# Optimization experiments

Hardware: AMD Instinct MI355X
Metric: run time of the kernel (lower is better)

Reference implementation:

```python
import jax, jax.numpy as jnp
import numpy as np
import math

B, T, F, H, C = 64, 128, 2048, 1024, 22

def setup_inputs() -> dict:
    key = jax.random.key(0)
    ks = jax.random.split(key, 16)
    def w(k, shape, fan_in):
        s = 1.0 / math.sqrt(fan_in)
        return jax.random.uniform(k, shape, jnp.float32, -s, s)
    return {
        "x": jax.random.normal(ks[0], (B, T, F), jnp.float32),
        # encoder LSTM (input F, hidden H); PyTorch gate order i,f,g,o
        "enc_Wih": w(ks[1], (4 * H, F), H),
        "enc_Whh": w(ks[2], (4 * H, H), H),
        "enc_bih": w(ks[3], (4 * H,), H),
        "enc_bhh": w(ks[4], (4 * H,), H),
        # enc->dec and dec->enc projections (both HxH, unidirectional)
        "We2d": w(ks[5], (H, H), H),
        "be2d": w(ks[6], (H,), H),
        "Wd2e": w(ks[7], (H, H), H),
        "bd2e": w(ks[8], (H,), H),
        # decoder LSTMCell (input F + H, hidden H)
        "dec_Wih": w(ks[9], (4 * H, F + H), H),
        "dec_Whh": w(ks[10], (4 * H, H), H),
        "dec_bih": w(ks[11], (4 * H,), H),
        "dec_bhh": w(ks[12], (4 * H,), H),
        # classifier
        "Wc": w(ks[13], (C, H), H),
        "bc": w(ks[14], (C,), H),
    }

def _lstm_cell(x_t, h, c, Wih, Whh, b):
    g = x_t @ Wih.T + h @ Whh.T + b  # [B, 4H]
    i, f, gg, o = jnp.split(g, 4, axis=-1)
    c_new = jax.nn.sigmoid(f) * c + jax.nn.sigmoid(i) * jnp.tanh(gg)
    h_new = jax.nn.sigmoid(o) * jnp.tanh(c_new)
    return h_new, c_new

def reference(x, enc_Wih, enc_Whh, enc_bih, enc_bhh, We2d, be2d, Wd2e, bd2e,
              dec_Wih, dec_Whh, dec_bih, dec_bhh, Wc, bc):
    Bx, Tx, _ = x.shape
    Hh = enc_Whh.shape[1]
    enc_b = enc_bih + enc_bhh
    dec_b = dec_bih + dec_bhh

    # ---- encoder LSTM over time (feature extractor is identity) ----
    xT = jnp.swapaxes(x, 0, 1)  # [T, B, F]
    def enc_step(carry, x_t):
        h, c = carry
        h, c = _lstm_cell(x_t, h, c, enc_Wih, enc_Whh, enc_b)
        return (h, c), h
    h0 = jnp.zeros((Bx, Hh), x.dtype)
    (_, _), h_ts = jax.lax.scan(enc_step, (h0, h0), xT)  # [T, B, H]
    h_ts = jnp.swapaxes(h_ts, 0, 1)  # [B, T, H]

    proj_h_ts = h_ts @ We2d.T + be2d  # [B, T, H]
    scale = 1.0 / math.sqrt(Hh)

    # ---- decoder with per-step attention ----
    def dec_step(carry, x_t):
        h, c = carry
        logits = jnp.einsum('bh,bth->bt', h, proj_h_ts) * scale
        aw = jax.nn.softmax(logits, axis=-1)           # [B, T]
        attn = jnp.einsum('bt,bth->bh', aw, proj_h_ts)  # [B, H]
        attn = attn @ Wd2e.T + bd2e
        inp = jnp.concatenate([x_t, attn], axis=-1)     # [B, F+H]
        h, c = _lstm_cell(inp, h, c, dec_Wih, dec_Whh, dec_b)
        sc = h @ Wc.T + bc                              # [B, C]
        return (h, c), (sc, aw)

    (_, _), (scores_T, aw_T) = jax.lax.scan(dec_step, (h0, h0), xT)
    scores = jnp.swapaxes(scores_T, 0, 1)  # [B, T, C]
    return scores, aw_T[-1]  # last step's attention weights [B, T]
```

## Files before the change

kernel.cpp:

```cpp
#include <hip/hip_runtime.h>
#include <hip/hip_bf16.h>

#define BB 64
#define TT 128
#define FF 2048
#define HH 1024
#define CC 22
#define G4 4096
#define KD 2048
#define BT 8192

typedef __attribute__((ext_vector_type(8))) short bf16x8;
typedef __attribute__((ext_vector_type(4))) float f32x4;

__device__ __forceinline__ f32x4 mfma16(bf16x8 a, bf16x8 b, f32x4 c) {
    return __builtin_amdgcn_mfma_f32_16x16x32_bf16(a, b, c, 0, 0, 0);
}

__device__ __forceinline__ float b2f(short s) {
    unsigned int u = ((unsigned int)(unsigned short)s) << 16;
    union { unsigned int i; float f; } x; x.i = u; return x.f;
}

__device__ __forceinline__ short f2bs(float f) {
    union { __hip_bfloat16 h; short s; } u;
    u.h = __float2bfloat16(f);
    return u.s;
}


__global__ void zero_u32(unsigned int* p, long long n) {
    long long i = (long long)blockIdx.x * 256 + threadIdx.x;
    if (i < n) p[i] = 0u;
}

__global__ void fill_f32(float* p, long long n, float v) {
    long long i = (long long)blockIdx.x * 256 + threadIdx.x;
    if (i < n) p[i] = v;
}

__global__ void pack_bf16(const float* __restrict__ src, long long sld, long long soff,
                          __hip_bfloat16* __restrict__ dst, long long dld,
                          int rows, int cols, int valid) {
    long long i = (long long)blockIdx.x * 256 + threadIdx.x;
    long long tot = (long long)rows * cols;
    if (i >= tot) return;
    int r = (int)(i / cols), c = (int)(i % cols);
    float v = (r < valid) ? src[(long long)r * sld + soff + c] : 0.f;
    dst[(long long)r * dld + c] = __float2bfloat16(v);
}

__global__ void packT_bf16(const float* __restrict__ src, int R, int Ccols,
                           __hip_bfloat16* __restrict__ dst) {
    long long i = (long long)blockIdx.x * 256 + threadIdx.x;
    long long tot = (long long)R * Ccols;
    if (i >= tot) return;
    int r = (int)(i / Ccols), c = (int)(i % Ccols);
    dst[(long long)c * R + r] = __float2bfloat16(src[i]);
}

__global__ void add_bias2(const float* a, const float* b, float* out, int n) {
    int i = blockIdx.x * 256 + threadIdx.x;
    if (i < n) out[i] = a[i] + b[i];
}

__global__ void pad_bias(const float* src, float* dst, int nsrc, int ndst) {
    int i = blockIdx.x * blockDim.x + threadIdx.x;
    if (i < ndst) dst[i] = (i < nsrc) ? src[i] : 0.f;
}

__global__ __launch_bounds__(64) void bcomb_kernel(const float* __restrict__ dWih,
                                                   const float* __restrict__ bd2e,
                                                   const float* __restrict__ dbih,
                                                   const float* __restrict__ dbhh,
                                                   float* __restrict__ badd) {
    int r = blockIdx.x, lane = threadIdx.x;
    const float* row = dWih + (long long)r * (FF + HH) + FF;
    float s = 0.f;
    for (int k = lane; k < HH; k += 64) s += row[k] * bd2e[k];
    #pragma unroll
    for (int off = 32; off; off >>= 1) s += __shfl_xor(s, off, 64);
    if (lane == 0) badd[r] = s + dbih[r] + dbhh[r];
}

template <int K, bool AF32>
__global__ __launch_bounds__(256) void gemm_tile(
    const void* __restrict__ Aptr, long long lda,
    const __hip_bfloat16* __restrict__ W,
    const float* __restrict__ bias, void* __restrict__ Cout, int out_bf16,
    long long ldc, int n_store) {
    int tid = threadIdx.x;
    int wave = tid >> 6, lane = tid & 63;
    int wm = wave >> 1, wn = wave & 1;
    int m_base = blockIdx.x * 128 + wm * 64;
    int n_base = blockIdx.y * 128 + wn * 64;
    int row_in = lane & 15, k8 = (lane >> 4) * 8;

    f32x4 acc[4][4] = {};
    const float* Af = (const float*)Aptr + (long long)(m_base + row_in) * lda + k8;
    const __hip_bfloat16* Ab = (const __hip_bfloat16*)Aptr + (long long)(m_base + row_in) * lda + k8;
    const __hip_bfloat16* Wp = W + (long long)(n_base + row_in) * K + k8;

    #pragma unroll 2
    for (int k0 = 0; k0 < K; k0 += 32) {
        bf16x8 a[4], b[4];
        #pragma unroll
        for (int i = 0; i < 4; i++) {
            if (AF32) {
                const float* p = Af + (long long)i * 16 * lda + k0;
                const float4 f0 = *(const float4*)(p);
                const float4 f1 = *(const float4*)(p + 4);
                a[i][0] = f2bs(f0.x); a[i][1] = f2bs(f0.y);
                a[i][2] = f2bs(f0.z); a[i][3] = f2bs(f0.w);
                a[i][4] = f2bs(f1.x); a[i][5] = f2bs(f1.y);
                a[i][6] = f2bs(f1.z); a[i][7] = f2bs(f1.w);
            } else {
                a[i] = *(const bf16x8*)(Ab + (long long)i * 16 * lda + k0);
            }
        }
        #pragma unroll
        for (int i = 0; i < 4; i++) b[i] = *(const bf16x8*)(Wp + (long long)i * 16 * K + k0);
        #pragma unroll
        for (int mt = 0; mt < 4; mt++)
            #pragma unroll
            for (int nt = 0; nt < 4; nt++)
                acc[mt][nt] = mfma16(a[mt], b[nt], acc[mt][nt]);
    }

    int col = lane & 15, rowq = (lane >> 4) * 4;
    #pragma unroll
    for (int mt = 0; mt < 4; mt++)
        #pragma unroll
        for (int nt = 0; nt < 4; nt++) {
            int n = n_base + nt * 16 + col;
            if (n >= n_store) continue;
            float bv = bias ? bias[n] : 0.f;
            #pragma unroll
            for (int r = 0; r < 4; r++) {
                long long m = m_base + mt * 16 + rowq + r;
                float v = acc[mt][nt][r] + bv;
                if (out_bf16) ((__hip_bfloat16*)Cout)[m * ldc + n] = __float2bfloat16(v);
                else          ((float*)Cout)[m * ldc + n] = v;
            }
        }
}

template <int KZ>
__global__ __launch_bounds__(1024) void fused_step(
    const __hip_bfloat16* __restrict__ Z,
    const __hip_bfloat16* __restrict__ W,
    const __hip_bfloat16* __restrict__ Xg_t, long long xg_stride,
    float* __restrict__ c,
    float* __restrict__ h_f32,
    __hip_bfloat16* __restrict__ hb_a, long long stride_a,
    __hip_bfloat16* __restrict__ hb_b, long long stride_b) {
    constexpr int KQ = KZ / 4;
    __shared__ float P[16 * 256];
    int tid = threadIdx.x;
    int wave = tid >> 6, lane = tid & 63;
    int g = wave >> 2, ks = wave & 3;
    int hh_t = blockIdx.x & 63, mb = blockIdx.x >> 6;
    int m_base = mb * 16;
    int hh0 = hh_t * 16;
    int n0 = g * HH + hh0;
    int row_in = lane & 15, k8 = (lane >> 4) * 8;
    long long koff = (long long)ks * KQ + k8;

    const __hip_bfloat16* Ap = Z + (long long)(m_base + row_in) * KZ + koff;
    const __hip_bfloat16* Wp = W + (long long)(n0 + row_in) * KZ + koff;

    f32x4 acc = {};
    #pragma unroll 8
    for (int k0 = 0; k0 < KQ; k0 += 32) {
        bf16x8 bw = *(const bf16x8*)(Wp + k0);
        bf16x8 a0 = *(const bf16x8*)(Ap + k0);
        acc = mfma16(a0, bw, acc);
    }

    int col = lane & 15, rowq = (lane >> 4) * 4;
    #pragma unroll
    for (int r = 0; r < 4; r++)
        P[wave * 256 + (rowq + r) * 16 + col] = acc[r];
    __syncthreads();

    if (tid < 256) {
        int bl = tid >> 4, hl = tid & 15;
        int bb = m_base + bl, hh = hh0 + hl;
        float gv[4];
        #pragma unroll
        for (int gg2 = 0; gg2 < 4; gg2++) {
            float s = 0.f;
            #pragma unroll
            for (int kk = 0; kk < 4; kk++) s += P[(gg2 * 4 + kk) * 256 + tid];
            gv[gg2] = s + __bfloat162float(Xg_t[(long long)bb * xg_stride + gg2 * HH + hh]);
        }
        float si = 1.f / (1.f + __expf(-gv[0]));
        float sf = 1.f / (1.f + __expf(-gv[1]));
        float tg = tanhf(gv[2]);
        float so = 1.f / (1.f + __expf(-gv[3]));
        long long idx = (long long)bb * HH + hh;
        float cn = sf * c[idx] + si * tg;
        c[idx] = cn;
        float hn = so * tanhf(cn);
        if (h_f32) h_f32[idx] = hn;
        __hip_bfloat16 hb = __float2bfloat16(hn);
        hb_a[(long long)bb * stride_a + hh] = hb;
        hb_b[(long long)bb * stride_b + hh] = hb;
    }
}

__global__ __launch_bounds__(1024) void attn_fused(
    const float* __restrict__ h_dec,
    const __hip_bfloat16* __restrict__ proj,
    __hip_bfloat16* __restrict__ Z,
    float* __restrict__ aw_out) {
    __shared__ float lsm[TT];
    __shared__ float red[2];
    __shared__ float osum[32 * 264];
    int bx = blockIdx.x;
    int b = bx & 63, hq = bx >> 6;
    int tid = threadIdx.x, wave = tid >> 6, lane = tid & 63;

    float hreg[16];
    const float* hp = h_dec + (long long)b * HH + lane * 16;
    #pragma unroll
    for (int j = 0; j < 16; j++) hreg[j] = hp[j];

    const __hip_bfloat16* pb = proj + (long long)b * TT * HH + lane * 16;
    const float scale = 0.03125f;

    #pragma unroll
    for (int i = 0; i < 8; i++) {
        int t = wave * 8 + i;
        const __hip_bfloat16* p = pb + (long long)t * HH;
        bf16x8 p0 = *(const bf16x8*)(p);
        bf16x8 p1 = *(const bf16x8*)(p + 8);
        float dot = 0.f;
        #pragma unroll
        for (int j = 0; j < 8; j++) dot += hreg[j] * b2f(p0[j]) + hreg[8 + j] * b2f(p1[j]);
        #pragma unroll
        for (int off = 32; off; off >>= 1) dot += __shfl_xor(dot, off, 64);
        if (lane == 0) lsm[t] = dot * scale;
    }
    __syncthreads();

    if (wave == 0) {
        float a = lsm[lane], c2 = lsm[lane + 64];
        float mx = fmaxf(a, c2);
        #pragma unroll
        for (int off = 32; off; off >>= 1) mx = fmaxf(mx, __shfl_xor(mx, off, 64));
        float s = __expf(a - mx) + __expf(c2 - mx);
        #pragma unroll
        for (int off = 32; off; off >>= 1) s += __shfl_xor(s, off, 64);
        if (lane == 0) { red[0] = mx; red[1] = s; }
    }
    __syncthreads();
    float mstar = red[0], invL = 1.f / red[1];

    int hw = tid & 31, tg = tid >> 5;
    const __hip_bfloat16* base = proj + (long long)b * TT * HH + hq * 256 + hw * 8;
    float o8[8];
    #pragma unroll
    for (int j = 0; j < 8; j++) o8[j] = 0.f;
    #pragma unroll
    for (int k = 0; k < 4; k++) {
        int t = tg + k * 32;
        float w = __expf(lsm[t] - mstar) * invL;
        bf16x8 p = *(const bf16x8*)(base + (long long)t * HH);
        #pragma unroll
        for (int j = 0; j < 8; j++) o8[j] += w * b2f(p[j]);
    }
    #pragma unroll
    for (int j = 0; j < 8; j++) osum[tg * 264 + hw * 8 + j] = o8[j];
    __syncthreads();

    if (tid < 256) {
        float s = 0.f;
        #pragma unroll
        for (int g2 = 0; g2 < 32; g2++) s += osum[g2 * 264 + tid];
        Z[(long long)b * KD + hq * 256 + tid] = __float2bfloat16(s);
    }
    if (aw_out && hq == 0 && tid < TT)
        aw_out[(long long)b * TT + tid] = __expf(lsm[tid] - mstar) * invL;
}


extern "C" void kernel_launch(void* const* d_in, const int* in_sizes, int n_in,
                              void* d_out, int out_size, void* d_ws, size_t ws_size,
                              hipStream_t stream) {
    const float* x    = (const float*)d_in[0];
    const float* eWih = (const float*)d_in[1];
    const float* eWhh = (const float*)d_in[2];
    const float* ebih = (const float*)d_in[3];
    const float* ebhh = (const float*)d_in[4];
    const float* We2d = (const float*)d_in[5];
    const float* be2d = (const float*)d_in[6];
    const float* Wd2e = (const float*)d_in[7];
    const float* bd2e = (const float*)d_in[8];
    const float* dWih = (const float*)d_in[9];
    const float* dWhh = (const float*)d_in[10];
    const float* dbih = (const float*)d_in[11];
    const float* dbhh = (const float*)d_in[12];
    const float* Wc   = (const float*)d_in[13];
    const float* bc   = (const float*)d_in[14];

    float* scores = (float*)d_out;
    float* aw_out = scores + (size_t)BB * TT * CC;

    char* ws = (char*)d_ws;
    size_t off = 0;
    auto alloc = [&](size_t bytes) -> char* {
        char* p = ws + off;
        off = (off + bytes + 255) & ~(size_t)255;
        return p;
    };

    __hip_bfloat16* Xg    = (__hip_bfloat16*)alloc((size_t)BT * G4 * 2);
    char*           Bz    = alloc((size_t)G4 * KD * 2);
    char*           Cp    = alloc((size_t)G4 * FF * 2);
    __hip_bfloat16* hts   = (__hip_bfloat16*)alloc((size_t)BT * HH * 2);
    __hip_bfloat16* Wd2eT = (__hip_bfloat16*)alloc((size_t)HH * HH * 2);
    __hip_bfloat16* We2dB = (__hip_bfloat16*)alloc((size_t)HH * HH * 2);
    __hip_bfloat16* WcP   = (__hip_bfloat16*)alloc((size_t)128 * HH * 2);
    float*          encb  = (float*)alloc((size_t)G4 * 4);
    float*          badd  = (float*)alloc((size_t)G4 * 4);
    float*          bcP   = (float*)alloc((size_t)128 * 4);
    char*           state = alloc(1572864);
    float*          cenc = (float*)(state);
    float*          cdec = (float*)(state + 262144);
    float*          hdec = (float*)(state + 524288);
    __hip_bfloat16* he0  = (__hip_bfloat16*)(state + 786432);
    __hip_bfloat16* he1  = (__hip_bfloat16*)(state + 917504);
    __hip_bfloat16* Zb0  = (__hip_bfloat16*)(state + 1048576);
    __hip_bfloat16* Zb1  = (__hip_bfloat16*)(state + 1310720);

    __hip_bfloat16* eWhhB = (__hip_bfloat16*)Bz;
    __hip_bfloat16* Wz    = (__hip_bfloat16*)Bz;
    __hip_bfloat16* eWihB = (__hip_bfloat16*)Cp;
    __hip_bfloat16* dWxB  = (__hip_bfloat16*)Cp;
    __hip_bfloat16* proj  = (__hip_bfloat16*)Cp;
    __hip_bfloat16* hdts  = hts;

    (void)in_sizes; (void)n_in;

    if (off > ws_size) {
        long long n = out_size;
        fill_f32<<<dim3((unsigned)((n + 255) / 256)), 256, 0, stream>>>((float*)d_out, n, 111.0f);
        return;
    }

    auto packGrid = [](long long tot) { return dim3((unsigned)((tot + 255) / 256)); };

    zero_u32<<<dim3(1536), dim3(256), 0, stream>>>((unsigned int*)state, 393216LL);
    pack_bf16<<<packGrid((long long)G4 * FF), 256, 0, stream>>>(eWih, FF, 0, eWihB, FF, G4, FF, G4);
    pack_bf16<<<packGrid((long long)G4 * HH), 256, 0, stream>>>(eWhh, HH, 0, eWhhB, HH, G4, HH, G4);
    packT_bf16<<<packGrid((long long)HH * HH), 256, 0, stream>>>(Wd2e, HH, HH, Wd2eT);
    pack_bf16<<<packGrid((long long)HH * HH), 256, 0, stream>>>(We2d, HH, 0, We2dB, HH, HH, HH, HH);
    pack_bf16<<<packGrid((long long)128 * HH), 256, 0, stream>>>(Wc, HH, 0, WcP, HH, 128, HH, CC);
    add_bias2<<<16, 256, 0, stream>>>(ebih, ebhh, encb, G4);
    pad_bias<<<1, 128, 0, stream>>>(bc, bcP, CC, 128);
    bcomb_kernel<<<G4, 64, 0, stream>>>(dWih, bd2e, dbih, dbhh, badd);

    gemm_tile<FF, true><<<dim3(BT / 128, G4 / 128), 256, 0, stream>>>(
        x, FF, eWihB, encb, Xg, 1, G4, G4);

    for (int t = 0; t < TT; t++) {
        __hip_bfloat16* hin  = (t & 1) ? he1 : he0;
        __hip_bfloat16* hout = (t & 1) ? he0 : he1;
        fused_step<HH><<<dim3(256), dim3(1024), 0, stream>>>(
            hin, eWhhB, Xg + (size_t)t * G4, (long long)TT * G4,
            cenc, nullptr, hout, HH, hts + (size_t)t * HH, (long long)TT * HH);
    }

    pack_bf16<<<packGrid((long long)G4 * FF), 256, 0, stream>>>(dWih, FF + HH, 0, dWxB, FF, G4, FF, G4);
    gemm_tile<FF, true><<<dim3(BT / 128, G4 / 128), 256, 0, stream>>>(
        x, FF, dWxB, badd, Xg, 1, G4, G4);

    gemm_tile<HH, true><<<dim3(G4 / 128, HH / 128), 256, 0, stream>>>(
        dWih + FF, FF + HH, Wd2eT, nullptr, Wz, 1, KD, HH);
    pack_bf16<<<packGrid((long long)G4 * HH), 256, 0, stream>>>(dWhh, HH, 0, Wz + HH, KD, G4, HH, G4);

    gemm_tile<HH, false><<<dim3(BT / 128, HH / 128), 256, 0, stream>>>(
        hts, HH, We2dB, be2d, proj, 1, HH, HH);

    for (int t = 0; t < TT; t++) {
        __hip_bfloat16* Zin  = (t & 1) ? Zb1 : Zb0;
        __hip_bfloat16* Znxt = (t & 1) ? Zb0 : Zb1;
        attn_fused<<<dim3(256), dim3(1024), 0, stream>>>(
            hdec, proj, Zin, (t == TT - 1) ? aw_out : nullptr);
        fused_step<KD><<<dim3(256), dim3(1024), 0, stream>>>(
            Zin, Wz, Xg + (size_t)t * G4, (long long)TT * G4,
            cdec, hdec, Znxt + HH, KD, hdts + (size_t)t * HH, (long long)TT * HH);
    }

    gemm_tile<HH, false><<<dim3(BT / 128, 1), 256, 0, stream>>>(
        hdts, HH, WcP, bcP, scores, 0, CC, CC);
}
```

Measured before the change: 6.466 ms.

## Split attention logits across blocks with flag sync; pre-convert x to bf16

Each of the four blocks per batch row now computes only its 32 time-step logits instead of recomputing all 128, publishes them to global memory, and waits on per-block flags for its three sibling blocks before doing the softmax. This removes fourfold redundant logit work per decoder step, at the cost of a spin-wait barrier between blocks that relies on all 256 blocks being co-resident. Separately, x is converted to bf16 once when workspace allows, and both input-projection GEMMs read the bf16 copy instead of converting fp32 on the fly.

```diff
diff --git a/kernel.cpp b/kernel.cpp
--- a/kernel.cpp
+++ b/kernel.cpp
@@ -209,10 +209,13 @@
     }
 }
 
-__global__ __launch_bounds__(1024) void attn_fused(
+__global__ __launch_bounds__(1024) void attn2(
     const float* __restrict__ h_dec,
     const __hip_bfloat16* __restrict__ proj,
+    float* __restrict__ logits_g,
     __hip_bfloat16* __restrict__ Z,
+    unsigned int* __restrict__ flags,
+    unsigned int want,
     float* __restrict__ aw_out) {
     __shared__ float lsm[TT];
     __shared__ float red[2];
@@ -230,8 +233,8 @@
     const float scale = 0.03125f;
 
     #pragma unroll
-    for (int i = 0; i < 8; i++) {
-        int t = wave * 8 + i;
+    for (int it = 0; it < 2; it++) {
+        int t = hq * 32 + wave * 2 + it;
         const __hip_bfloat16* p = pb + (long long)t * HH;
         bf16x8 p0 = *(const bf16x8*)(p);
         bf16x8 p1 = *(const bf16x8*)(p + 8);
@@ -240,8 +243,28 @@
         for (int j = 0; j < 8; j++) dot += hreg[j] * b2f(p0[j]) + hreg[8 + j] * b2f(p1[j]);
         #pragma unroll
         for (int off = 32; off; off >>= 1) dot += __shfl_xor(dot, off, 64);
-        if (lane == 0) lsm[t] = dot * scale;
-    }
+        if (lane == 0) {
+            float lv = dot * scale;
+            lsm[t] = lv;
+            __hip_atomic_store((float*)&logits_g[b * TT + t], lv,
+                               __ATOMIC_RELAXED, __HIP_MEMORY_SCOPE_AGENT);
+        }
+    }
+    __syncthreads();
+
+    if (tid == 0)
+        __hip_atomic_store(&flags[bx], want, __ATOMIC_RELEASE, __HIP_MEMORY_SCOPE_AGENT);
+    if (tid < 3) {
+        int q2 = (hq + 1 + tid) & 3;
+        const unsigned int* fp = flags + b + 64 * q2;
+        while (__hip_atomic_load(fp, __ATOMIC_ACQUIRE, __HIP_MEMORY_SCOPE_AGENT) < want)
+            __builtin_amdgcn_s_sleep(1);
+    }
+    __syncthreads();
+
+    if (tid < TT && (tid >> 5) != hq)
+        lsm[tid] = __hip_atomic_load((const float*)&logits_g[b * TT + tid],
+                                     __ATOMIC_RELAXED, __HIP_MEMORY_SCOPE_AGENT);
     __syncthreads();
 
     if (wave == 0) {
@@ -325,7 +348,7 @@
     float*          encb  = (float*)alloc((size_t)G4 * 4);
     float*          badd  = (float*)alloc((size_t)G4 * 4);
     float*          bcP   = (float*)alloc((size_t)128 * 4);
-    char*           state = alloc(1572864);
+    char*           state = alloc(1572864 + 32768 + 1024);
     float*          cenc = (float*)(state);
     float*          cdec = (float*)(state + 262144);
     float*          hdec = (float*)(state + 524288);
@@ -333,6 +356,8 @@
     __hip_bfloat16* he1  = (__hip_bfloat16*)(state + 917504);
     __hip_bfloat16* Zb0  = (__hip_bfloat16*)(state + 1048576);
     __hip_bfloat16* Zb1  = (__hip_bfloat16*)(state + 1310720);
+    float*          logits_g = (float*)(state + 1572864);
+    unsigned int*   dflags   = (unsigned int*)(state + 1572864 + 32768);
 
     __hip_bfloat16* eWhhB = (__hip_bfloat16*)Bz;
     __hip_bfloat16* Wz    = (__hip_bfloat16*)Bz;
@@ -349,9 +374,14 @@
         return;
     }
 
+    __hip_bfloat16* xB = nullptr;
+    if (off + (size_t)BT * FF * 2 <= ws_size) {
+        xB = (__hip_bfloat16*)(ws + off);
+    }
+
     auto packGrid = [](long long tot) { return dim3((unsigned)((tot + 255) / 256)); };
 
-    zero_u32<<<dim3(1536), dim3(256), 0, stream>>>((unsigned int*)state, 393216LL);
+    zero_u32<<<dim3(1569), dim3(256), 0, stream>>>((unsigned int*)state, 401664LL);
     pack_bf16<<<packGrid((long long)G4 * FF), 256, 0, stream>>>(eWih, FF, 0, eWihB, FF, G4, FF, G4);
     pack_bf16<<<packGrid((long long)G4 * HH), 256, 0, stream>>>(eWhh, HH, 0, eWhhB, HH, G4, HH, G4);
     packT_bf16<<<packGrid((long long)HH * HH), 256, 0, stream>>>(Wd2e, HH, HH, Wd2eT);
@@ -360,9 +390,15 @@
     add_bias2<<<16, 256, 0, stream>>>(ebih, ebhh, encb, G4);
     pad_bias<<<1, 128, 0, stream>>>(bc, bcP, CC, 128);
     bcomb_kernel<<<G4, 64, 0, stream>>>(dWih, bd2e, dbih, dbhh, badd);
-
-    gemm_tile<FF, true><<<dim3(BT / 128, G4 / 128), 256, 0, stream>>>(
-        x, FF, eWihB, encb, Xg, 1, G4, G4);
+    if (xB)
+        pack_bf16<<<packGrid((long long)BT * FF), 256, 0, stream>>>(x, FF, 0, xB, FF, BT, FF, BT);
+
+    if (xB)
+        gemm_tile<FF, false><<<dim3(BT / 128, G4 / 128), 256, 0, stream>>>(
+            xB, FF, eWihB, encb, Xg, 1, G4, G4);
+    else
+        gemm_tile<FF, true><<<dim3(BT / 128, G4 / 128), 256, 0, stream>>>(
+            x, FF, eWihB, encb, Xg, 1, G4, G4);
 
     for (int t = 0; t < TT; t++) {
         __hip_bfloat16* hin  = (t & 1) ? he1 : he0;
@@ -373,8 +409,12 @@
     }
 
     pack_bf16<<<packGrid((long long)G4 * FF), 256, 0, stream>>>(dWih, FF + HH, 0, dWxB, FF, G4, FF, G4);
-    gemm_tile<FF, true><<<dim3(BT / 128, G4 / 128), 256, 0, stream>>>(
-        x, FF, dWxB, badd, Xg, 1, G4, G4);
+    if (xB)
+        gemm_tile<FF, false><<<dim3(BT / 128, G4 / 128), 256, 0, stream>>>(
+            xB, FF, dWxB, badd, Xg, 1, G4, G4);
+    else
+        gemm_tile<FF, true><<<dim3(BT / 128, G4 / 128), 256, 0, stream>>>(
+            x, FF, dWxB, badd, Xg, 1, G4, G4);
 
     gemm_tile<HH, true><<<dim3(G4 / 128, HH / 128), 256, 0, stream>>>(
         dWih + FF, FF + HH, Wd2eT, nullptr, Wz, 1, KD, HH);
@@ -386,8 +426,9 @@
     for (int t = 0; t < TT; t++) {
         __hip_bfloat16* Zin  = (t & 1) ? Zb1 : Zb0;
         __hip_bfloat16* Znxt = (t & 1) ? Zb0 : Zb1;
-        attn_fused<<<dim3(256), dim3(1024), 0, stream>>>(
-            hdec, proj, Zin, (t == TT - 1) ? aw_out : nullptr);
+        attn2<<<dim3(256), dim3(1024), 0, stream>>>(
+            hdec, proj, logits_g, Zin, dflags, (unsigned)(t + 1),
+            (t == TT - 1) ? aw_out : nullptr);
         fused_step<KD><<<dim3(256), dim3(1024), 0, stream>>>(
             Zin, Wz, Xg + (size_t)t * G4, (long long)TT * G4,
             cdec, hdec, Znxt + HH, KD, hdts + (size_t)t * HH, (long long)TT * HH);
```

After: 6.838 ms. 5.8% more time.
